# Kernel tuning notes

Measured on AMD Instinct MI355X. Metric: run time of the kernel, lower is better.

## Reference

```python
import jax, jax.numpy as jnp
import numpy as np

N = 20        # number_of_nodes
K = 2         # Chebyshev order
E_DIM = 4     # embedding_dimensions
OUT = 2       # out_channels
F_IN = 8      # node_features
B = 131072    # batch


def setup_inputs() -> dict:
    key = jax.random.key(0)
    ks = jax.random.split(key, 8)
    x = jax.random.normal(ks[0], (B, N, F_IN), jnp.float32)
    e = jax.random.normal(ks[1], (N, E_DIM), jnp.float32)
    # AVWGCN parameter pools: weights_pool (E_DIM, K, in, out), bias_pool (E_DIM, out)
    gate_w = jax.random.normal(ks[2], (E_DIM, K, F_IN + OUT, 2 * OUT), jnp.float32) * 0.1
    gate_b = jax.random.normal(ks[3], (E_DIM, 2 * OUT), jnp.float32) * 0.1
    upd_w = jax.random.normal(ks[4], (E_DIM, K, F_IN + OUT, OUT), jnp.float32) * 0.1
    upd_b = jax.random.normal(ks[5], (E_DIM, OUT), jnp.float32) * 0.1
    lin_w = jax.random.normal(ks[6], (1, OUT), jnp.float32) * 0.5
    lin_b = jax.random.normal(ks[7], (1,), jnp.float32) * 0.1
    return {"x": x, "e": e, "gate_w": gate_w, "gate_b": gate_b,
            "upd_w": upd_w, "upd_b": upd_b, "lin_w": lin_w, "lin_b": lin_b}


def _avwgcn(x, e, supports, w_pool, b_pool):
    # Node-adaptive weights: (N, K, in, out) and bias (N, out)
    W = jnp.einsum('nd,dkio->nkio', e, w_pool)
    b = e @ b_pool
    # K-hop graph conv gather: (B, N, K, in)
    x_g = jnp.einsum('knm,bmc->bnkc', supports, x)
    return jnp.einsum('bnki,nkio->bno', x_g, W) + b


def reference(x, e, gate_w, gate_b, upd_w, upd_b, lin_w, lin_b):
    dt = x.dtype
    # Adaptive adjacency: softmax(relu(E E^T)) rows; Chebyshev set for K=2 is [I, A]
    A = jax.nn.softmax(jax.nn.relu(e @ e.T), axis=1)
    supports = jnp.stack([jnp.eye(N, dtype=dt), A.astype(dt)])  # (K, N, N)

    H = jnp.zeros((x.shape[0], N, OUT), dt)  # self.h is None -> zeros
    XH = jnp.concatenate([x, H], axis=-1)
    ZR = jax.nn.sigmoid(_avwgcn(XH, e, supports, gate_w, gate_b))
    Z, R = ZR[..., :OUT], ZR[..., OUT:]
    C = jnp.concatenate([x, Z * H], axis=-1)
    HC = jnp.tanh(_avwgcn(C, e, supports, upd_w, upd_b))
    H = R * H + (1.0 - R) * HC

    y = jax.nn.relu(H)
    y = y @ lin_w.T + lin_b
    return y
```

## Files before the change

kernel.cpp:

```cpp
#include <hip/hip_runtime.h>
#include <math.h>

#define NN 20
#define ED 4
#define XROW 160
#define NC 80
#define NKT 5
#define NNT 5
#define FRAG_BYTES (NKT * NNT * 64 * 16)
#define THREADS 512
#define ROWS_PER_WAVE 16
#define ROWS_PER_BLOCK 128
#define TPB 2

typedef __attribute__((ext_vector_type(8))) _Float16 half8;
typedef __attribute__((ext_vector_type(4))) float f32x4;
typedef __attribute__((ext_vector_type(4))) unsigned uint4v;

static __device__ __forceinline__ half8 cvt8(float4 a, float4 b) {
    uint4v u = (uint4v){
        __builtin_bit_cast(unsigned, __builtin_amdgcn_cvt_pkrtz(a.x, a.y)),
        __builtin_bit_cast(unsigned, __builtin_amdgcn_cvt_pkrtz(a.z, a.w)),
        __builtin_bit_cast(unsigned, __builtin_amdgcn_cvt_pkrtz(b.x, b.y)),
        __builtin_bit_cast(unsigned, __builtin_amdgcn_cvt_pkrtz(b.z, b.w))};
    return __builtin_bit_cast(half8, u);
}

static __device__ __forceinline__ float dpp_xor1(float v) {
    return __builtin_bit_cast(float,
        __builtin_amdgcn_mov_dpp(__builtin_bit_cast(int, v), 0xB1, 0xF, 0xF, true));
}
static __device__ __forceinline__ float dpp_xor2(float v) {
    return __builtin_bit_cast(float,
        __builtin_amdgcn_mov_dpp(__builtin_bit_cast(int, v), 0x4E, 0xF, 0xF, true));
}

#define BARRIER_NODRAIN()                                   \
    do {                                                    \
        asm volatile("s_waitcnt lgkmcnt(0)" ::: "memory");  \
        __builtin_amdgcn_s_barrier();                       \
        __builtin_amdgcn_sched_barrier(0);                  \
    } while (0)

struct Burst {
    float4 a0, b0, a1, b1, a2, b2, a3, b3, a4, b4;
};

static __device__ __forceinline__ Burst load_burst(const float* __restrict__ p) {
    Burst r;
    r.a0 = *(const float4*)(p);       r.b0 = *(const float4*)(p + 4);
    r.a1 = *(const float4*)(p + 32);  r.b1 = *(const float4*)(p + 36);
    r.a2 = *(const float4*)(p + 64);  r.b2 = *(const float4*)(p + 68);
    r.a3 = *(const float4*)(p + 96);  r.b3 = *(const float4*)(p + 100);
    r.a4 = *(const float4*)(p + 128); r.b4 = *(const float4*)(p + 132);
    return r;
}

__global__ __launch_bounds__(THREADS, 4) void rgcn_fused(
        const float* __restrict__ x,
        const float* __restrict__ e,
        const float* __restrict__ gate_w,
        const float* __restrict__ gate_b,
        const float* __restrict__ upd_w,
        const float* __restrict__ upd_b,
        const float* __restrict__ lin_w,
        const float* __restrict__ lin_b,
        float* __restrict__ y) {
    __shared__ __align__(16) char fragmem[FRAG_BYTES];
    __shared__ float sbias[NC];
    __shared__ float el[80];
    __shared__ float sA[400];
    __shared__ float wself[640];
    __shared__ float wagg[640];

    const int t = threadIdx.x;
    const int l = t & 63;
    const int w = t >> 6;

    const size_t rowA = ((size_t)blockIdx.x * TPB + 0) * ROWS_PER_BLOCK + (size_t)w * ROWS_PER_WAVE;
    const size_t rowB = ((size_t)blockIdx.x * TPB + 1) * ROWS_PER_BLOCK + (size_t)w * ROWS_PER_WAVE;
    const float* xpA = x + (rowA + (l & 15)) * XROW + ((l >> 4) << 3);
    const float* xpB = x + (rowB + (l & 15)) * XROW + ((l >> 4) << 3);

    const float lw0 = lin_w[0], lw1 = lin_w[1], lb = lin_b[0];

    float ev = 0.f;
    if (t < NN * ED) ev = e[t];

    float q0a[ED], q1a[ED];
    {
        int c = t >> 3, i = t & 7, ro = c & 3;
        const float* b0; const float* b1; int st;
        if (ro < 2) { b0 = gate_w + i * 4 + 2 + ro; b1 = b0 + 40; st = 80; }
        else        { b0 = upd_w  + i * 2 + ro - 2; b1 = b0 + 20; st = 40; }
        #pragma unroll
        for (int d = 0; d < ED; ++d) { q0a[d] = b0[d * st]; q1a[d] = b1[d * st]; }
    }
    float q0b[ED], q1b[ED];
    if (t < 128) {
        int rem = t + 512;
        int c = rem >> 3, i = rem & 7, ro = c & 3;
        const float* b0; const float* b1; int st;
        if (ro < 2) { b0 = gate_w + i * 4 + 2 + ro; b1 = b0 + 40; st = 80; }
        else        { b0 = upd_w  + i * 2 + ro - 2; b1 = b0 + 20; st = 40; }
        #pragma unroll
        for (int d = 0; d < ED; ++d) { q0b[d] = b0[d * st]; q1b[d] = b1[d * st]; }
    }
    float pb[ED];
    if (t < NC) {
        int rb = t & 3;
        #pragma unroll
        for (int d = 0; d < ED; ++d)
            pb[d] = (rb < 2) ? gate_b[d * 4 + 2 + rb] : upd_b[d * 2 + rb - 2];
    }

    Burst bA = load_burst(xpA);
    Burst bB = load_burst(xpB);
    __builtin_amdgcn_sched_barrier(0);

    if (t < NN * ED) el[t] = ev;
    BARRIER_NODRAIN();

    if (t < 400) {
        int nn = t / 20, mm = t - (t / 20) * 20;
        float d = 0.f;
        #pragma unroll
        for (int j = 0; j < ED; ++j) d += el[nn * ED + j] * el[mm * ED + j];
        sA[t] = fmaxf(d, 0.f);
    }
    {
        int n1 = t >> 5;
        float vs = 0.f, va = 0.f;
        #pragma unroll
        for (int d = 0; d < ED; ++d) {
            float evd = el[n1 * ED + d];
            vs += evd * q0a[d];
            va += evd * q1a[d];
        }
        wself[t] = vs;
        wagg[t]  = va;
    }
    if (t < 128) {
        int rem = t + 512, n2 = rem >> 5;
        float vs = 0.f, va = 0.f;
        #pragma unroll
        for (int d = 0; d < ED; ++d) {
            float evd = el[n2 * ED + d];
            vs += evd * q0b[d];
            va += evd * q1b[d];
        }
        wself[rem] = vs;
        wagg[rem]  = va;
    }
    if (t < NC) {
        float b = 0.f;
        #pragma unroll
        for (int d = 0; d < ED; ++d) b += el[(t >> 2) * ED + d] * pb[d];
        sbias[t] = b;
    }
    BARRIER_NODRAIN();

    if (t < NN) {
        float mx = -1e30f;
        for (int m = 0; m < NN; ++m) mx = fmaxf(mx, sA[t * 20 + m]);
        float ex[NN]; float sum = 0.f;
        for (int m = 0; m < NN; ++m) { ex[m] = __expf(sA[t * 20 + m] - mx); sum += ex[m]; }
        float inv = 1.f / sum;
        for (int m = 0; m < NN; ++m) sA[t * 20 + m] = ex[m] * inv;
    }
    BARRIER_NODRAIN();

    {
        half8* frag = (half8*)fragmem;
        for (int tile = w; tile < NKT * NNT; tile += 8) {
            int kt = tile / 5, nt = tile - kt * 5;
            int cc = nt * 16 + (l & 15);
            int nn = cc >> 2;
            int mm = kt * 4 + (l >> 4);
            float anm = sA[nn * 20 + mm];
            float4 wg0 = *(const float4*)&wagg[cc * 8];
            float4 wg1 = *(const float4*)&wagg[cc * 8 + 4];
            float v0 = anm * wg0.x, v1 = anm * wg0.y, v2 = anm * wg0.z, v3 = anm * wg0.w;
            float v4 = anm * wg1.x, v5 = anm * wg1.y, v6 = anm * wg1.z, v7 = anm * wg1.w;
            if (nn == mm) {
                float4 ws0 = *(const float4*)&wself[cc * 8];
                float4 ws1 = *(const float4*)&wself[cc * 8 + 4];
                v0 += ws0.x; v1 += ws0.y; v2 += ws0.z; v3 += ws0.w;
                v4 += ws1.x; v5 += ws1.y; v6 += ws1.z; v7 += ws1.w;
            }
            half8 hv;
            hv[0] = (_Float16)v0; hv[1] = (_Float16)v1; hv[2] = (_Float16)v2; hv[3] = (_Float16)v3;
            hv[4] = (_Float16)v4; hv[5] = (_Float16)v5; hv[6] = (_Float16)v6; hv[7] = (_Float16)v7;
            frag[tile * 64 + l] = hv;
        }
    }
    BARRIER_NODRAIN();

    const half8* frag = (const half8*)fragmem;
    const int ro = l & 3;
    const bool isR = ro < 2;
    const float myw = (ro & 1) ? lw1 : lw0;

    #define STEP(XA, XB, KT, ACC)                                                   \
    {                                                                               \
        half8 a = cvt8(XA, XB);                                                     \
        _Pragma("unroll")                                                           \
        for (int nt = 0; nt < NNT; ++nt) {                                          \
            half8 bh = frag[((KT) * NNT + nt) * 64 + l];                            \
            ACC[nt] = __builtin_amdgcn_mfma_f32_16x16x32_f16(a, bh, ACC[nt], 0, 0, 0); \
        }                                                                           \
    }

    #define EPILOGUE(ACC, ROW0)                                                     \
    {                                                                               \
        const size_t rowb = (ROW0) + ((l >> 4) << 2) + ro;                          \
        _Pragma("unroll")                                                           \
        for (int nt = 0; nt < NNT; ++nt) {                                          \
            const int n = nt * 4 + ((l & 15) >> 2);                                 \
            float ysel = 0.f;                                                       \
            _Pragma("unroll")                                                       \
            for (int q = 0; q < 4; ++q) {                                           \
                float pre = ACC[nt][q];                                             \
                float term;                                                         \
                if (isR) term = __builtin_amdgcn_rcpf(1.f + __expf(pre));           \
                else     term = 1.f - 2.f * __builtin_amdgcn_rcpf(__expf(2.f * pre) + 1.f); \
                float other = dpp_xor2(term);                                       \
                float h = term * other;                                             \
                float s = fmaxf(h, 0.f) * myw;                                      \
                float yq = s + dpp_xor1(s) + lb;                                    \
                if (q == ro) ysel = yq;                                             \
            }                                                                       \
            y[rowb * NN + n] = ysel;                                                \
        }                                                                           \
    }

    {
        f32x4 accA[NNT];
        #pragma unroll
        for (int nt = 0; nt < NNT; ++nt) {
            float b = sbias[nt * 16 + (l & 15)];
            accA[nt] = (f32x4){b, b, b, b};
        }
        STEP(bA.a0, bA.b0, 0, accA)
        STEP(bA.a1, bA.b1, 1, accA)
        STEP(bA.a2, bA.b2, 2, accA)
        STEP(bA.a3, bA.b3, 3, accA)
        STEP(bA.a4, bA.b4, 4, accA)
        EPILOGUE(accA, rowA)
    }

    {
        f32x4 accB[NNT];
        #pragma unroll
        for (int nt = 0; nt < NNT; ++nt) {
            float b = sbias[nt * 16 + (l & 15)];
            accB[nt] = (f32x4){b, b, b, b};
        }
        STEP(bB.a0, bB.b0, 0, accB)
        STEP(bB.a1, bB.b1, 1, accB)
        STEP(bB.a2, bB.b2, 2, accB)
        STEP(bB.a3, bB.b3, 3, accB)
        STEP(bB.a4, bB.b4, 4, accB)
        EPILOGUE(accB, rowB)
    }
    #undef STEP
    #undef EPILOGUE
}

extern "C" void kernel_launch(void* const* d_in, const int* in_sizes, int n_in,
                              void* d_out, int out_size, void* d_ws, size_t ws_size,
                              hipStream_t stream) {
    const float* x      = (const float*)d_in[0];
    const float* e      = (const float*)d_in[1];
    const float* gate_w = (const float*)d_in[2];
    const float* gate_b = (const float*)d_in[3];
    const float* upd_w  = (const float*)d_in[4];
    const float* upd_b  = (const float*)d_in[5];
    const float* lin_w  = (const float*)d_in[6];
    const float* lin_b  = (const float*)d_in[7];
    float* y = (float*)d_out;

    const int Bn = in_sizes[0] / XROW;
    const int nblocks = Bn / (ROWS_PER_BLOCK * TPB);

    rgcn_fused<<<nblocks, THREADS, 0, stream>>>(x, e, gate_w, gate_b,
                                                upd_w, upd_b, lin_w, lin_b, y);
}
```

Measured before the change: 25.20 us.

## Split per-block weight/adjacency setup into a single-block prologue kernel via workspace

Moves the adjacency softmax, node-adaptive weight synthesis and MFMA fragment packing out of every main-kernel block into a one-block setup kernel. That kernel writes the packed fragments, bias and linear params to the workspace, and the main kernel only copies them into LDS. It also turns the serial per-row softmax into a wave-shuffle reduction. This removes redundant per-block prologue work and two barriers, but adds a second kernel launch with a serial dependency and a global round-trip for the constants.

```diff
diff --git a/kernel.cpp b/kernel.cpp
--- a/kernel.cpp
+++ b/kernel.cpp
@@ -8,7 +8,12 @@
 #define NKT 5
 #define NNT 5
 #define FRAG_BYTES (NKT * NNT * 64 * 16)
+#define BIAS_OFF   FRAG_BYTES
+#define LIN_OFF    (BIAS_OFF + NC * 4)
+#define CONS_BYTES (LIN_OFF + 16)
+#define CONS_U4    (CONS_BYTES / 16)
 #define THREADS 512
+#define STH 640
 #define ROWS_PER_WAVE 16
 #define ROWS_PER_BLOCK 128
 #define TPB 2
@@ -34,13 +39,6 @@
     return __builtin_bit_cast(float,
         __builtin_amdgcn_mov_dpp(__builtin_bit_cast(int, v), 0x4E, 0xF, 0xF, true));
 }
-
-#define BARRIER_NODRAIN()                                   \
-    do {                                                    \
-        asm volatile("s_waitcnt lgkmcnt(0)" ::: "memory");  \
-        __builtin_amdgcn_s_barrier();                       \
-        __builtin_amdgcn_sched_barrier(0);                  \
-    } while (0)
 
 struct Burst {
     float4 a0, b0, a1, b1, a2, b2, a3, b3, a4, b4;
@@ -56,8 +54,7 @@
     return r;
 }
 
-__global__ __launch_bounds__(THREADS, 4) void rgcn_fused(
-        const float* __restrict__ x,
+__global__ __launch_bounds__(STH) void rgcn_setup(
         const float* __restrict__ e,
         const float* __restrict__ gate_w,
         const float* __restrict__ gate_b,
@@ -65,14 +62,110 @@
         const float* __restrict__ upd_b,
         const float* __restrict__ lin_w,
         const float* __restrict__ lin_b,
-        float* __restrict__ y) {
-    __shared__ __align__(16) char fragmem[FRAG_BYTES];
-    __shared__ float sbias[NC];
+        char* __restrict__ ws) {
     __shared__ float el[80];
     __shared__ float sA[400];
     __shared__ float wself[640];
     __shared__ float wagg[640];
-
+    const int t = threadIdx.x;
+    const int l = t & 63;
+    const int w = t >> 6;
+
+    const int c = t >> 3, i = t & 7, ro = c & 3;
+    const int n_ = c >> 2;
+    float p0[ED], p1[ED];
+    {
+        const float* b0; const float* b1; int st;
+        if (ro < 2) { b0 = gate_w + i * 4 + 2 + ro; b1 = b0 + 40; st = 80; }
+        else        { b0 = upd_w  + i * 2 + ro - 2; b1 = b0 + 20; st = 40; }
+        #pragma unroll
+        for (int d = 0; d < ED; ++d) { p0[d] = b0[d * st]; p1[d] = b1[d * st]; }
+    }
+    float pb[ED];
+    if (t < NC) {
+        int rb = t & 3;
+        #pragma unroll
+        for (int d = 0; d < ED; ++d)
+            pb[d] = (rb < 2) ? gate_b[d * 4 + 2 + rb] : upd_b[d * 2 + rb - 2];
+    }
+    if (t < 80) el[t] = e[t];
+    float* wbias = (float*)(ws + BIAS_OFF);
+    float* wlin  = (float*)(ws + LIN_OFF);
+    if (t == 0) { wlin[0] = lin_w[0]; wlin[1] = lin_w[1]; wlin[2] = lin_b[0]; wlin[3] = 0.f; }
+    __syncthreads();
+
+    if (t < 400) {
+        int nn = t / 20, mm = t - (t / 20) * 20;
+        float d = 0.f;
+        #pragma unroll
+        for (int j = 0; j < ED; ++j) d += el[nn * ED + j] * el[mm * ED + j];
+        sA[t] = fmaxf(d, 0.f);
+    }
+    {
+        float vs = 0.f, va = 0.f;
+        #pragma unroll
+        for (int d = 0; d < ED; ++d) {
+            float evd = el[n_ * ED + d];
+            vs += evd * p0[d];
+            va += evd * p1[d];
+        }
+        wself[t] = vs;
+        wagg[t]  = va;
+    }
+    if (t < NC) {
+        float b = 0.f;
+        #pragma unroll
+        for (int d = 0; d < ED; ++d) b += el[(t >> 2) * ED + d] * pb[d];
+        wbias[t] = b;
+    }
+    __syncthreads();
+
+    #pragma unroll
+    for (int rep = 0; rep < 2; ++rep) {
+        int r = w + rep * 10;
+        if (r < NN) {
+            float v = (l < NN) ? sA[r * 20 + l] : -1e30f;
+            float mx = v;
+            #pragma unroll
+            for (int s = 32; s >= 1; s >>= 1) mx = fmaxf(mx, __shfl_xor(mx, s));
+            float ex = (l < NN) ? __expf(v - mx) : 0.f;
+            float sum = ex;
+            #pragma unroll
+            for (int s = 32; s >= 1; s >>= 1) sum += __shfl_xor(sum, s);
+            if (l < NN) sA[r * 20 + l] = ex / sum;
+        }
+    }
+    __syncthreads();
+
+    half8* frag = (half8*)ws;
+    for (int tile = w; tile < NKT * NNT; tile += (STH / 64)) {
+        int kt = tile / 5, nt = tile - kt * 5;
+        int cc = nt * 16 + (l & 15);
+        int nn = cc >> 2;
+        int mm = kt * 4 + (l >> 4);
+        float anm = sA[nn * 20 + mm];
+        float4 wg0 = *(const float4*)&wagg[cc * 8];
+        float4 wg1 = *(const float4*)&wagg[cc * 8 + 4];
+        float v0 = anm * wg0.x, v1 = anm * wg0.y, v2 = anm * wg0.z, v3 = anm * wg0.w;
+        float v4 = anm * wg1.x, v5 = anm * wg1.y, v6 = anm * wg1.z, v7 = anm * wg1.w;
+        if (nn == mm) {
+            float4 ws0 = *(const float4*)&wself[cc * 8];
+            float4 ws1 = *(const float4*)&wself[cc * 8 + 4];
+            v0 += ws0.x; v1 += ws0.y; v2 += ws0.z; v3 += ws0.w;
+            v4 += ws1.x; v5 += ws1.y; v6 += ws1.z; v7 += ws1.w;
+        }
+        half8 hv;
+        hv[0] = (_Float16)v0; hv[1] = (_Float16)v1; hv[2] = (_Float16)v2; hv[3] = (_Float16)v3;
+        hv[4] = (_Float16)v4; hv[5] = (_Float16)v5; hv[6] = (_Float16)v6; hv[7] = (_Float16)v7;
+        frag[tile * 64 + l] = hv;
+    }
+}
+
+__global__ __launch_bounds__(THREADS, 4) void rgcn_main(
+        const float* __restrict__ x,
+        const char* __restrict__ cons,
+        float* __restrict__ y) {
+    __shared__ __align__(16) char smem[CONS_BYTES];
     const int t = threadIdx.x;
     const int l = t & 63;
     const int w = t >> 6;
@@ -82,121 +175,21 @@
     const float* xpA = x + (rowA + (l & 15)) * XROW + ((l >> 4) << 3);
     const float* xpB = x + (rowB + (l & 15)) * XROW + ((l >> 4) << 3);
 
-    const float lw0 = lin_w[0], lw1 = lin_w[1], lb = lin_b[0];
-
-    float ev = 0.f;
-    if (t < NN * ED) ev = e[t];
-
-    float q0a[ED], q1a[ED];
-    {
-        int c = t >> 3, i = t & 7, ro = c & 3;
-        const float* b0; const float* b1; int st;
-        if (ro < 2) { b0 = gate_w + i * 4 + 2 + ro; b1 = b0 + 40; st = 80; }
-        else        { b0 = upd_w  + i * 2 + ro - 2; b1 = b0 + 20; st = 40; }
-        #pragma unroll
-        for (int d = 0; d < ED; ++d) { q0a[d] = b0[d * st]; q1a[d] = b1[d * st]; }
-    }
-    float q0b[ED], q1b[ED];
-    if (t < 128) {
-        int rem = t + 512;
-        int c = rem >> 3, i = rem & 7, ro = c & 3;
-        const float* b0; const float* b1; int st;
-        if (ro < 2) { b0 = gate_w + i * 4 + 2 + ro; b1 = b0 + 40; st = 80; }
-        else        { b0 = upd_w  + i * 2 + ro - 2; b1 = b0 + 20; st = 40; }
-        #pragma unroll
-        for (int d = 0; d < ED; ++d) { q0b[d] = b0[d * st]; q1b[d] = b1[d * st]; }
-    }
-    float pb[ED];
-    if (t < NC) {
-        int rb = t & 3;
-        #pragma unroll
-        for (int d = 0; d < ED; ++d)
-            pb[d] = (rb < 2) ? gate_b[d * 4 + 2 + rb] : upd_b[d * 2 + rb - 2];
-    }
-
     Burst bA = load_burst(xpA);
     Burst bB = load_burst(xpB);
-    __builtin_amdgcn_sched_barrier(0);
-
-    if (t < NN * ED) el[t] = ev;
-    BARRIER_NODRAIN();
-
-    if (t < 400) {
-        int nn = t / 20, mm = t - (t / 20) * 20;
-        float d = 0.f;
-        #pragma unroll
-        for (int j = 0; j < ED; ++j) d += el[nn * ED + j] * el[mm * ED + j];
-        sA[t] = fmaxf(d, 0.f);
-    }
-    {
-        int n1 = t >> 5;
-        float vs = 0.f, va = 0.f;
-        #pragma unroll
-        for (int d = 0; d < ED; ++d) {
-            float evd = el[n1 * ED + d];
-            vs += evd * q0a[d];
-            va += evd * q1a[d];
-        }
-        wself[t] = vs;
-        wagg[t]  = va;
-    }
-    if (t < 128) {
-        int rem = t + 512, n2 = rem >> 5;
-        float vs = 0.f, va = 0.f;
-        #pragma unroll
-        for (int d = 0; d < ED; ++d) {
-            float evd = el[n2 * ED + d];
-            vs += evd * q0b[d];
-            va += evd * q1b[d];
-        }
-        wself[rem] = vs;
-        wagg[rem]  = va;
-    }
-    if (t < NC) {
-        float b = 0.f;
-        #pragma unroll
-        for (int d = 0; d < ED; ++d) b += el[(t >> 2) * ED + d] * pb[d];
-        sbias[t] = b;
-    }
-    BARRIER_NODRAIN();
-
-    if (t < NN) {
-        float mx = -1e30f;
-        for (int m = 0; m < NN; ++m) mx = fmaxf(mx, sA[t * 20 + m]);
-        float ex[NN]; float sum = 0.f;
-        for (int m = 0; m < NN; ++m) { ex[m] = __expf(sA[t * 20 + m] - mx); sum += ex[m]; }
-        float inv = 1.f / sum;
-        for (int m = 0; m < NN; ++m) sA[t * 20 + m] = ex[m] * inv;
-    }
-    BARRIER_NODRAIN();
-
-    {
-        half8* frag = (half8*)fragmem;
-        for (int tile = w; tile < NKT * NNT; tile += 8) {
-            int kt = tile / 5, nt = tile - kt * 5;
-            int cc = nt * 16 + (l & 15);
-            int nn = cc >> 2;
-            int mm = kt * 4 + (l >> 4);
-            float anm = sA[nn * 20 + mm];
-            float4 wg0 = *(const float4*)&wagg[cc * 8];
-            float4 wg1 = *(const float4*)&wagg[cc * 8 + 4];
-            float v0 = anm * wg0.x, v1 = anm * wg0.y, v2 = anm * wg0.z, v3 = anm * wg0.w;
-            float v4 = anm * wg1.x, v5 = anm * wg1.y, v6 = anm * wg1.z, v7 = anm * wg1.w;
-            if (nn == mm) {
-                float4 ws0 = *(const float4*)&wself[cc * 8];
-                float4 ws1 = *(const float4*)&wself[cc * 8 + 4];
-                v0 += ws0.x; v1 += ws0.y; v2 += ws0.z; v3 += ws0.w;
-                v4 += ws1.x; v5 += ws1.y; v6 += ws1.z; v7 += ws1.w;
-            }
-            half8 hv;
-            hv[0] = (_Float16)v0; hv[1] = (_Float16)v1; hv[2] = (_Float16)v2; hv[3] = (_Float16)v3;
-            hv[4] = (_Float16)v4; hv[5] = (_Float16)v5; hv[6] = (_Float16)v6; hv[7] = (_Float16)v7;
-            frag[tile * 64 + l] = hv;
-        }
-    }
-    BARRIER_NODRAIN();
-
-    const half8* frag = (const half8*)fragmem;
+
+    {
+        const uint4v* src = (const uint4v*)cons;
+        uint4v* dst = (uint4v*)smem;
+        #pragma unroll
+        for (int i = t; i < CONS_U4; i += THREADS) dst[i] = src[i];
+    }
+    __syncthreads();
+
+    const half8* frag = (const half8*)smem;
+    const float* sbias = (const float*)(smem + BIAS_OFF);
+    const float* slin  = (const float*)(smem + LIN_OFF);
+    const float lw0 = slin[0], lw1 = slin[1], lb = slin[2];
     const int ro = l & 3;
     const bool isR = ro < 2;
     const float myw = (ro & 1) ? lw1 : lw0;
@@ -248,7 +241,6 @@
         STEP(bA.a4, bA.b4, 4, accA)
         EPILOGUE(accA, rowA)
     }
-
     {
         f32x4 accB[NNT];
         #pragma unroll
@@ -278,11 +270,13 @@
     const float* upd_b  = (const float*)d_in[5];
     const float* lin_w  = (const float*)d_in[6];
     const float* lin_b  = (const float*)d_in[7];
-    float* y = (float*)d_out;
+    char* cons = (char*)d_ws;
+    float* y   = (float*)d_out;
 
     const int Bn = in_sizes[0] / XROW;
     const int nblocks = Bn / (ROWS_PER_BLOCK * TPB);
 
-    rgcn_fused<<<nblocks, THREADS, 0, stream>>>(x, e, gate_w, gate_b,
-                                                upd_w, upd_b, lin_w, lin_b, y);
-}
+    rgcn_setup<<<1, STH, 0, stream>>>(e, gate_w, gate_b, upd_w, upd_b,
+                                      lin_w, lin_b, cons);
+    rgcn_main<<<nblocks, THREADS, 0, stream>>>(x, cons, y);
+}
```

Measured after the change: 28.65 us. 1.14x slower.

## Process four row tiles per block with staggered x loads; parallelize softmax

Applied to the files above, without the earlier changes.

Each block now handles four 128-row tiles instead of two. Tiles two and three are loaded while the first tiles are being computed, so the per-block setup (adjacency, weight generation, fragment build) is amortised over more rows and global loads overlap MFMA work. The adjacency row softmax moves from 20 serial threads to wave-level shuffle reductions. Launch bounds drop to 2 blocks per CU, which raises register headroom for the extra in-flight bursts but halves the block count and may reduce occupancy and tail balance.

```diff
diff --git a/kernel.cpp b/kernel.cpp
--- a/kernel.cpp
+++ b/kernel.cpp
@@ -10,8 +10,9 @@
 #define FRAG_BYTES (NKT * NNT * 64 * 16)
 #define THREADS 512
 #define ROWS_PER_WAVE 16
-#define ROWS_PER_BLOCK 128
-#define TPB 2
+#define TILE_ROWS 128
+#define TPB 4
+#define ROWS_PER_BLOCK (TILE_ROWS * TPB)
 
 typedef __attribute__((ext_vector_type(8))) _Float16 half8;
 typedef __attribute__((ext_vector_type(4))) float f32x4;
@@ -56,7 +57,7 @@
     return r;
 }
 
-__global__ __launch_bounds__(THREADS, 4) void rgcn_fused(
+__global__ __launch_bounds__(THREADS, 2) void rgcn_fused(
         const float* __restrict__ x,
         const float* __restrict__ e,
         const float* __restrict__ gate_w,
@@ -77,16 +78,16 @@
     const int l = t & 63;
     const int w = t >> 6;
 
-    const size_t rowA = ((size_t)blockIdx.x * TPB + 0) * ROWS_PER_BLOCK + (size_t)w * ROWS_PER_WAVE;
-    const size_t rowB = ((size_t)blockIdx.x * TPB + 1) * ROWS_PER_BLOCK + (size_t)w * ROWS_PER_WAVE;
-    const float* xpA = x + (rowA + (l & 15)) * XROW + ((l >> 4) << 3);
-    const float* xpB = x + (rowB + (l & 15)) * XROW + ((l >> 4) << 3);
+    const size_t base = (size_t)blockIdx.x * ROWS_PER_BLOCK + (size_t)w * ROWS_PER_WAVE;
+    const float* xp0 = x + (base + (l & 15)) * XROW + ((l >> 4) << 3);
+    const float* xp1 = xp0 + (size_t)TILE_ROWS * XROW;
+    const float* xp2 = xp1 + (size_t)TILE_ROWS * XROW;
+    const float* xp3 = xp2 + (size_t)TILE_ROWS * XROW;
 
     const float lw0 = lin_w[0], lw1 = lin_w[1], lb = lin_b[0];
 
     float ev = 0.f;
     if (t < NN * ED) ev = e[t];
-
     float q0a[ED], q1a[ED];
     {
         int c = t >> 3, i = t & 7, ro = c & 3;
@@ -113,9 +114,10 @@
         for (int d = 0; d < ED; ++d)
             pb[d] = (rb < 2) ? gate_b[d * 4 + 2 + rb] : upd_b[d * 2 + rb - 2];
     }
-
-    Burst bA = load_burst(xpA);
-    Burst bB = load_burst(xpB);
+    __builtin_amdgcn_sched_barrier(0);
+
+    Burst bA = load_burst(xp0);
+    Burst bB = load_burst(xp1);
     __builtin_amdgcn_sched_barrier(0);
 
     if (t < NN * ED) el[t] = ev;
@@ -160,13 +162,20 @@
     }
     BARRIER_NODRAIN();
 
-    if (t < NN) {
-        float mx = -1e30f;
-        for (int m = 0; m < NN; ++m) mx = fmaxf(mx, sA[t * 20 + m]);
-        float ex[NN]; float sum = 0.f;
-        for (int m = 0; m < NN; ++m) { ex[m] = __expf(sA[t * 20 + m] - mx); sum += ex[m]; }
-        float inv = 1.f / sum;
-        for (int m = 0; m < NN; ++m) sA[t * 20 + m] = ex[m] * inv;
+    #pragma unroll
+    for (int rep = 0; rep < 3; ++rep) {
+        int r = w + rep * 8;
+        if (r < NN) {
+            float v = (l < NN) ? sA[r * 20 + l] : -1e30f;
+            float mx = v;
+            #pragma unroll
+            for (int s = 32; s >= 1; s >>= 1) mx = fmaxf(mx, __shfl_xor(mx, s));
+            float ex = (l < NN) ? __expf(v - mx) : 0.f;
+            float sum = ex;
+            #pragma unroll
+            for (int s = 32; s >= 1; s >>= 1) sum += __shfl_xor(sum, s);
+            if (l < NN) sA[r * 20 + l] = ex / sum;
+        }
     }
     BARRIER_NODRAIN();
 
@@ -211,8 +220,19 @@
         }                                                                           \
     }
 
-    #define EPILOGUE(ACC, ROW0)                                                     \
+    #define COMPUTE(U, ROW0)                                                        \
     {                                                                               \
+        f32x4 acc[NNT];                                                             \
+        _Pragma("unroll")                                                           \
+        for (int nt = 0; nt < NNT; ++nt) {                                          \
+            float b = sbias[nt * 16 + (l & 15)];                                    \
+            acc[nt] = (f32x4){b, b, b, b};                                          \
+        }                                                                           \
+        STEP(U.a0, U.b0, 0, acc)                                                    \
+        STEP(U.a1, U.b1, 1, acc)                                                    \
+        STEP(U.a2, U.b2, 2, acc)                                                    \
+        STEP(U.a3, U.b3, 3, acc)                                                    \
+        STEP(U.a4, U.b4, 4, acc)                                                    \
         const size_t rowb = (ROW0) + ((l >> 4) << 2) + ro;                          \
         _Pragma("unroll")                                                           \
         for (int nt = 0; nt < NNT; ++nt) {                                          \
@@ -220,7 +240,7 @@
             float ysel = 0.f;                                                       \
             _Pragma("unroll")                                                       \
             for (int q = 0; q < 4; ++q) {                                           \
-                float pre = ACC[nt][q];                                             \
+                float pre = acc[nt][q];                                             \
                 float term;                                                         \
                 if (isR) term = __builtin_amdgcn_rcpf(1.f + __expf(pre));           \
                 else     term = 1.f - 2.f * __builtin_amdgcn_rcpf(__expf(2.f * pre) + 1.f); \
@@ -234,37 +254,16 @@
         }                                                                           \
     }
 
-    {
-        f32x4 accA[NNT];
-        #pragma unroll
-        for (int nt = 0; nt < NNT; ++nt) {
-            float b = sbias[nt * 16 + (l & 15)];
-            accA[nt] = (f32x4){b, b, b, b};
-        }
-        STEP(bA.a0, bA.b0, 0, accA)
-        STEP(bA.a1, bA.b1, 1, accA)
-        STEP(bA.a2, bA.b2, 2, accA)
-        STEP(bA.a3, bA.b3, 3, accA)
-        STEP(bA.a4, bA.b4, 4, accA)
-        EPILOGUE(accA, rowA)
-    }
-
-    {
-        f32x4 accB[NNT];
-        #pragma unroll
-        for (int nt = 0; nt < NNT; ++nt) {
-            float b = sbias[nt * 16 + (l & 15)];
-            accB[nt] = (f32x4){b, b, b, b};
-        }
-        STEP(bB.a0, bB.b0, 0, accB)
-        STEP(bB.a1, bB.b1, 1, accB)
-        STEP(bB.a2, bB.b2, 2, accB)
-        STEP(bB.a3, bB.b3, 3, accB)
-        STEP(bB.a4, bB.b4, 4, accB)
-        EPILOGUE(accB, rowB)
-    }
+    Burst bC = load_burst(xp2);
+    __builtin_amdgcn_sched_barrier(0);
+    COMPUTE(bA, base)
+    Burst bD = load_burst(xp3);
+    __builtin_amdgcn_sched_barrier(0);
+    COMPUTE(bB, base + TILE_ROWS)
+    COMPUTE(bC, base + 2 * TILE_ROWS)
+    COMPUTE(bD, base + 3 * TILE_ROWS)
     #undef STEP
-    #undef EPILOGUE
+    #undef COMPUTE
 }
 
 extern "C" void kernel_launch(void* const* d_in, const int* in_sizes, int n_in,
@@ -281,8 +280,7 @@
     float* y = (float*)d_out;
 
     const int Bn = in_sizes[0] / XROW;
-    const int nblocks = Bn / (ROWS_PER_BLOCK * TPB);
-
+    const int nblocks = Bn / ROWS_PER_BLOCK;
     rgcn_fused<<<nblocks, THREADS, 0, stream>>>(x, e, gate_w, gate_b,
                                                 upd_w, upd_b, lin_w, lin_b, y);
 }
```

Result: slower. 26.88 us (+6.7%).
